# Kernel optimization log

Hardware: AMD Instinct MI355X
Metric: run time of the kernel (lower is better)

## Reference

```python
import jax, jax.numpy as jnp
import numpy as np

N_NODES = 50000
N_EDGES = 800000
IN_DIM = 128
HID = 64
HEADS = 4
OUT_DIM = 64
NEG_SLOPE = 0.2


def setup_inputs() -> dict:
    key = jax.random.key(0)
    ks = jax.random.split(key, 12)
    x = jax.random.normal(ks[0], (N_NODES, IN_DIM), dtype=jnp.float32)
    edge_index = jax.random.randint(ks[1], (2, N_EDGES), 0, N_NODES, dtype=jnp.int64)
    s = 0.1
    # GATConv layer 1: in_dim -> hid per head, 4 heads, concat
    W1 = jax.random.normal(ks[2], (IN_DIM, HEADS * HID), dtype=jnp.float32) * s
    a_src1 = jax.random.normal(ks[3], (HEADS, HID), dtype=jnp.float32) * s
    a_dst1 = jax.random.normal(ks[4], (HEADS, HID), dtype=jnp.float32) * s
    b1 = jnp.zeros((HEADS * HID,), dtype=jnp.float32)
    # GATConv layer 2: hid*heads -> out_dim, 1 head
    W2 = jax.random.normal(ks[5], (HEADS * HID, OUT_DIM), dtype=jnp.float32) * s
    a_src2 = jax.random.normal(ks[6], (1, OUT_DIM), dtype=jnp.float32) * s
    a_dst2 = jax.random.normal(ks[7], (1, OUT_DIM), dtype=jnp.float32) * s
    b2 = jnp.zeros((OUT_DIM,), dtype=jnp.float32)
    # final linear out_dim -> 1
    fc_w = jax.random.normal(ks[8], (OUT_DIM, 1), dtype=jnp.float32) * s
    fc_b = jnp.zeros((1,), dtype=jnp.float32)
    return {"x": x, "edge_index": edge_index, "W1": W1, "a_src1": a_src1,
            "a_dst1": a_dst1, "b1": b1, "W2": W2, "a_src2": a_src2,
            "a_dst2": a_dst2, "b2": b2, "fc_w": fc_w, "fc_b": fc_b}


def _gat_layer(x, src, dst, W, a_src, a_dst, bias, heads, out_c):
    """PyG-style GATConv: gather, edge attention, segment softmax, scatter-sum."""
    n = x.shape[0]
    h = (x @ W).reshape(n, heads, out_c)                    # [N,H,C]
    alpha_s = jnp.sum(h * a_src, axis=-1)                   # [N,H]
    alpha_d = jnp.sum(h * a_dst, axis=-1)                   # [N,H]
    e = jax.nn.leaky_relu(alpha_s[src] + alpha_d[dst], NEG_SLOPE)  # [E,H]
    # segment softmax over incoming edges of each destination node
    m = jax.ops.segment_max(e, dst, num_segments=n)         # [N,H]
    ex = jnp.exp(e - m[dst])
    den = jax.ops.segment_sum(ex, dst, num_segments=n)      # [N,H]
    alpha = ex / (den[dst] + 1e-16)                         # [E,H]
    out = jax.ops.segment_sum(alpha[:, :, None] * h[src], dst, num_segments=n)
    return out.reshape(n, heads * out_c) + bias


def reference(x, edge_index, W1, a_src1, a_dst1, b1, W2, a_src2, a_dst2, b2, fc_w, fc_b):
    n = x.shape[0]
    # GATConv default add_self_loops=True
    loop = jnp.arange(n, dtype=edge_index.dtype)
    src = jnp.concatenate([edge_index[0], loop])
    dst = jnp.concatenate([edge_index[1], loop])
    h = _gat_layer(x, src, dst, W1, a_src1, a_dst1, b1, HEADS, HID)
    h = jax.nn.elu(h)
    h = _gat_layer(h, src, dst, W2, a_src2, a_dst2, b2, 1, OUT_DIM)
    return jnp.squeeze(h @ fc_w + fc_b)                      # [N]
```

## Files before the change

### kernel.cpp

```cpp
#include <hip/hip_runtime.h>
#include <hip/hip_fp16.h>

#define N_NODES 50000
#define N_EDGES 800000
#define E_TOT   850000
#define IN_DIM  128
#define HID     64
#define HEADS   4
#define C1      256
#define OUT_DIM 64
#define NEG_SLOPE 0.2f

#define CP_NODES   32
#define CP_BLOCKS  ((N_NODES + CP_NODES - 1) / CP_NODES)
#define COUNT_BLOCKS ((E_TOT + 255) / 256)
#define NB_SCAN ((N_NODES + 255) / 256)

typedef __attribute__((ext_vector_type(8))) short v8s;
typedef __attribute__((ext_vector_type(4))) float v4f;

__device__ __forceinline__ unsigned int bf16_rne(float f) {
    unsigned int u = __float_as_uint(f);
    return (u + 0x7FFFu + ((u >> 16) & 1u)) >> 16;
}
__device__ __forceinline__ unsigned int bf16_pack2(float a, float b) {
    return bf16_rne(a) | (bf16_rne(b) << 16);
}
__device__ __forceinline__ float bf16_lo(unsigned int u) { return __uint_as_float(u << 16); }
__device__ __forceinline__ float bf16_hi(unsigned int u) { return __uint_as_float(u & 0xFFFF0000u); }

__device__ __forceinline__ unsigned int f16_pack2(float a, float b) {
    __half2 h = __floats2half2_rn(a, b);
    return *(unsigned int*)&h;
}
__device__ __forceinline__ float2 f16_unp2(unsigned int u) {
    __half2 h = *(__half2*)&u;
    return __half22float2(h);
}

__global__ __launch_bounds__(512) void prep_kernel(
    const float* __restrict__ W1, const float* __restrict__ a_src1,
    const float* __restrict__ a_dst1,
    const float* __restrict__ W2, const float* __restrict__ a_src2,
    const float* __restrict__ a_dst2, const float* __restrict__ b2,
    const float* __restrict__ fc_w, const float* __restrict__ fc_b,
    float* __restrict__ p_src, float* __restrict__ p_dst,
    float* __restrict__ v_s, float* __restrict__ v_d, float* __restrict__ v_z,
    float* __restrict__ cst, unsigned int* __restrict__ W1b)
{
    const int t = threadIdx.x;
    if (blockIdx.x > 0) {
        int idx = (blockIdx.x - 1) * 512 + t;
        int i    = idx & 3;
        int lane = (idx >> 2) & 63;
        int kk   = (idx >> 8) & 3;
        int nt   = (idx >> 10) & 3;
        int hh   = idx >> 12;
        int k0 = kk * 32 + (lane >> 4) * 8 + i * 2;
        int c  = hh * 64 + nt * 16 + (lane & 15);
        W1b[idx] = bf16_pack2(W1[(size_t)k0 * C1 + c], W1[(size_t)(k0 + 1) * C1 + c]);
        return;
    }
    const int k = t >> 2, h = t & 3;
    const float* wrow = W1 + k * C1 + h * HID;
    const float* as = a_src1 + h * HID;
    const float* ad = a_dst1 + h * HID;
    float s = 0.f, d = 0.f;
    for (int c = 0; c < HID; c++) {
        float w = wrow[c];
        s = fmaf(w, as[c], s);
        d = fmaf(w, ad[c], d);
    }
    p_src[k * HEADS + h] = s;
    p_dst[k * HEADS + h] = d;

    if (t < C1) {
        const float* w2row = W2 + t * OUT_DIM;
        float vs = 0.f, vd = 0.f, vz = 0.f;
        for (int c = 0; c < OUT_DIM; c++) {
            float w = w2row[c];
            vs = fmaf(w, a_src2[c], vs);
            vd = fmaf(w, a_dst2[c], vd);
            vz = fmaf(w, fc_w[c], vz);
        }
        v_s[t] = vs; v_d[t] = vd; v_z[t] = vz;
    }
    if (t == 0) {
        float s2 = 0.f;
        for (int c = 0; c < OUT_DIM; c++) s2 = fmaf(b2[c], fc_w[c], s2);
        cst[0] = s2 + fc_b[0];
    }
}

__global__ __launch_bounds__(256) void convproj_count_kernel(
    const float* __restrict__ x, const float* __restrict__ p_src,
    const float* __restrict__ p_dst, const int* __restrict__ dst_a,
    float* __restrict__ as1, float* __restrict__ ad1,
    unsigned int* __restrict__ xb, int* __restrict__ deg,
    int* __restrict__ posE)
{
    if (blockIdx.x >= CP_BLOCKS) {
        int j = (blockIdx.x - CP_BLOCKS) * 256 + threadIdx.x;
        if (j < E_TOT) {
            int d = (j < N_EDGES) ? dst_a[j] : (j - N_EDGES);
            posE[j] = atomicAdd(&deg[d], 1);
        }
        return;
    }
    __shared__ float ps[IN_DIM * HEADS];
    __shared__ float pd[IN_DIM * HEADS];
    const int t = threadIdx.x;
    for (int i = t; i < IN_DIM * HEADS; i += 256) { ps[i] = p_src[i]; pd[i] = p_dst[i]; }
    __syncthreads();
    const int wv   = t >> 6;
    const int lane = t & 63;
    float4 p0 = *(const float4*)(ps + (lane * 2) * HEADS);
    float4 p1 = *(const float4*)(ps + (lane * 2 + 1) * HEADS);
    float4 q0 = *(const float4*)(pd + (lane * 2) * HEADS);
    float4 q1 = *(const float4*)(pd + (lane * 2 + 1) * HEADS);
    const int nodeBase = blockIdx.x * CP_NODES + wv * 8;
    #pragma unroll
    for (int i = 0; i < 8; i++) {
        const int node = nodeBase + i;
        if (node >= N_NODES) break;
        float2 xv = *(const float2*)(x + (size_t)node * IN_DIM + lane * 2);
        xb[(size_t)node * 64 + lane] = bf16_pack2(xv.x, xv.y);
        float s0 = xv.x * p0.x + xv.y * p1.x;
        float s1 = xv.x * p0.y + xv.y * p1.y;
        float s2 = xv.x * p0.z + xv.y * p1.z;
        float s3 = xv.x * p0.w + xv.y * p1.w;
        float d0 = xv.x * q0.x + xv.y * q1.x;
        float d1 = xv.x * q0.y + xv.y * q1.y;
        float d2 = xv.x * q0.z + xv.y * q1.z;
        float d3 = xv.x * q0.w + xv.y * q1.w;
        #pragma unroll
        for (int off = 32; off; off >>= 1) {
            s0 += __shfl_down(s0, off, 64); s1 += __shfl_down(s1, off, 64);
            s2 += __shfl_down(s2, off, 64); s3 += __shfl_down(s3, off, 64);
            d0 += __shfl_down(d0, off, 64); d1 += __shfl_down(d1, off, 64);
            d2 += __shfl_down(d2, off, 64); d3 += __shfl_down(d3, off, 64);
        }
        if (lane == 0) {
            float4 sv = {s0, s1, s2, s3};
            float4 dv = {d0, d1, d2, d3};
            *(float4*)(as1 + node * 4) = sv;
            *(float4*)(ad1 + node * 4) = dv;
        }
    }
}

__global__ __launch_bounds__(256) void scanfuse_kernel(
    const int* __restrict__ deg, int* __restrict__ rowptr,
    int* aggP, int* incP)
{
    __shared__ int ps[256];
    __shared__ int bs[256];
    __shared__ int sprev;
    const int t = threadIdx.x;
    const int b = blockIdx.x;
    int i = b * 256 + t;
    int v = (i < N_NODES) ? deg[i] : 0;
    ps[t] = v;
    __syncthreads();
    for (int off = 1; off < 256; off <<= 1) {
        int u = (t >= off) ? ps[t - off] : 0;
        __syncthreads();
        ps[t] += u;
        __syncthreads();
    }
    if (t == 255) atomicExch(&aggP[b], ps[255] + 1);
    if (b == 0) {
        int val = 0;
        if (t < NB_SCAN) {
            while ((val = atomicAdd(&aggP[t], 0)) == 0) {}
            val -= 1;
        }
        bs[t] = (t < NB_SCAN) ? val : 0;
        __syncthreads();
        for (int off = 1; off < 256; off <<= 1) {
            int u = (t >= off) ? bs[t - off] : 0;
            __syncthreads();
            bs[t] += u;
            __syncthreads();
        }
        if (t < NB_SCAN) atomicExch(&incP[t], (bs[t] - val) + 1);
    }
    if (t == 0) {
        int val;
        while ((val = atomicAdd(&incP[b], 0)) == 0) {}
        sprev = val - 1;
    }
    __syncthreads();
    if (i <= N_NODES) rowptr[i] = sprev + ps[t] - v;
}

__global__ void fillw3_kernel(const int* __restrict__ src_a, const int* __restrict__ dst_a,
                              const int* __restrict__ rowptr, const int* __restrict__ posE,
                              const float* __restrict__ as1, const float* __restrict__ ad1,
                              int4* __restrict__ rec)
{
    int j = blockIdx.x * blockDim.x + threadIdx.x;
    if (j >= E_TOT) return;
    int s, d;
    if (j < N_EDGES) { s = src_a[j]; d = dst_a[j]; }
    else             { s = j - N_EDGES; d = s; }
    int slot = rowptr[d] + posE[j];
    float4 A  = *(const float4*)(as1 + s * 4);
    float4 Dv = *(const float4*)(ad1 + d * 4);
    float a0 = A.x + Dv.x, a1 = A.y + Dv.y, a2 = A.z + Dv.z, a3 = A.w + Dv.w;
    a0 = a0 > 0.f ? a0 : NEG_SLOPE * a0;
    a1 = a1 > 0.f ? a1 : NEG_SLOPE * a1;
    a2 = a2 > 0.f ? a2 : NEG_SLOPE * a2;
    a3 = a3 > 0.f ? a3 : NEG_SLOPE * a3;
    int4 r;
    r.x = s;
    r.y = (int)f16_pack2(__expf(a0), __expf(a1));
    r.z = (int)f16_pack2(__expf(a2), __expf(a3));
    r.w = 0;
    rec[slot] = r;
}

__global__ __launch_bounds__(256, 4) void agg1mlp_kernel(
    const int* __restrict__ rowptr, const int4* __restrict__ rec,
    const unsigned int* __restrict__ xb,
    const unsigned int* __restrict__ W1b, const float* __restrict__ b1,
    const float* __restrict__ v_s, const float* __restrict__ v_d,
    const float* __restrict__ v_z,
    float2* __restrict__ az, float* __restrict__ ad2)
{
    __shared__ unsigned int xsh[16 * 260];
    __shared__ float pr[4 * 16 * 3];
    const int t = threadIdx.x;
    const int nodeBase = blockIdx.x * 16;
    const int wv   = t >> 6;
    const int lane = t & 63;

    #pragma unroll 1
    for (int i = 0; i < 4; i++) {
        const int ln = wv * 4 + i;
        const int n  = nodeBase + ln;
        const int e0 = rowptr[n], e1 = rowptr[n + 1];

        float2 acc0 = {0,0}, acc1 = {0,0}, acc2 = {0,0}, acc3 = {0,0};
        float den0 = 0, den1 = 0, den2 = 0, den3 = 0;
        int e = e0;

        #pragma unroll 1
        for (; e + 8 <= e1; e += 8) {
            int4 r[8];
            #pragma unroll
            for (int k = 0; k < 8; k++) r[k] = rec[e + k];
            unsigned int xu[8];
            #pragma unroll
            for (int k = 0; k < 8; k++)
                xu[k] = xb[((unsigned)r[k].x << 6) + lane];
            #pragma unroll
            for (int k = 0; k < 8; k++) {
                float2 Wa = f16_unp2(r[k].y), Wb = f16_unp2(r[k].z);
                float xa = bf16_lo(xu[k]), xbv = bf16_hi(xu[k]);
                acc0.x = fmaf(Wa.x, xa, acc0.x); acc0.y = fmaf(Wa.x, xbv, acc0.y);
                acc1.x = fmaf(Wa.y, xa, acc1.x); acc1.y = fmaf(Wa.y, xbv, acc1.y);
                acc2.x = fmaf(Wb.x, xa, acc2.x); acc2.y = fmaf(Wb.x, xbv, acc2.y);
                acc3.x = fmaf(Wb.y, xa, acc3.x); acc3.y = fmaf(Wb.y, xbv, acc3.y);
                den0 += Wa.x; den1 += Wa.y; den2 += Wb.x; den3 += Wb.y;
            }
        }
        if (e + 4 <= e1) {
            int4 r[4];
            #pragma unroll
            for (int k = 0; k < 4; k++) r[k] = rec[e + k];
            unsigned int xu[4];
            #pragma unroll
            for (int k = 0; k < 4; k++)
                xu[k] = xb[((unsigned)r[k].x << 6) + lane];
            #pragma unroll
            for (int k = 0; k < 4; k++) {
                float2 Wa = f16_unp2(r[k].y), Wb = f16_unp2(r[k].z);
                float xa = bf16_lo(xu[k]), xbv = bf16_hi(xu[k]);
                acc0.x = fmaf(Wa.x, xa, acc0.x); acc0.y = fmaf(Wa.x, xbv, acc0.y);
                acc1.x = fmaf(Wa.y, xa, acc1.x); acc1.y = fmaf(Wa.y, xbv, acc1.y);
                acc2.x = fmaf(Wb.x, xa, acc2.x); acc2.y = fmaf(Wb.x, xbv, acc2.y);
                acc3.x = fmaf(Wb.y, xa, acc3.x); acc3.y = fmaf(Wb.y, xbv, acc3.y);
                den0 += Wa.x; den1 += Wa.y; den2 += Wb.x; den3 += Wb.y;
            }
            e += 4;
        }
        for (; e < e1; e++) {
            int4 r0 = rec[e];
            unsigned int xu = xb[((unsigned)r0.x << 6) + lane];
            float2 Wa = f16_unp2(r0.y), Wb = f16_unp2(r0.z);
            float xa = bf16_lo(xu), xbv = bf16_hi(xu);
            acc0.x = fmaf(Wa.x, xa, acc0.x); acc0.y = fmaf(Wa.x, xbv, acc0.y);
            acc1.x = fmaf(Wa.y, xa, acc1.x); acc1.y = fmaf(Wa.y, xbv, acc1.y);
            acc2.x = fmaf(Wb.x, xa, acc2.x); acc2.y = fmaf(Wb.x, xbv, acc2.y);
            acc3.x = fmaf(Wb.y, xa, acc3.x); acc3.y = fmaf(Wb.y, xbv, acc3.y);
            den0 += Wa.x; den1 += Wa.y; den2 += Wb.x; den3 += Wb.y;
        }
        float i0 = 1.f / (den0 + 1e-16f), i1 = 1.f / (den1 + 1e-16f);
        float i2 = 1.f / (den2 + 1e-16f), i3 = 1.f / (den3 + 1e-16f);
        unsigned int* o = xsh + ln * 260 + lane;
        o[0 * 64] = bf16_pack2(acc0.x * i0, acc0.y * i0);
        o[1 * 64] = bf16_pack2(acc1.x * i1, acc1.y * i1);
        o[2 * 64] = bf16_pack2(acc2.x * i2, acc2.y * i2);
        o[3 * 64] = bf16_pack2(acc3.x * i3, acc3.y * i3);
    }
    __syncthreads();

    {
        const int h = wv;
        const int m = lane & 15, quad = lane >> 4;
        const unsigned int* abase = xsh + m * 260 + h * 64 + quad * 4;
        v8s af0 = *(const v8s*)(abase + 0);
        v8s af1 = *(const v8s*)(abase + 16);
        v8s af2 = *(const v8s*)(abase + 32);
        v8s af3 = *(const v8s*)(abase + 48);

        float Sr[4] = {0,0,0,0}, Dr[4] = {0,0,0,0}, Zr[4] = {0,0,0,0};
        #pragma unroll
        for (int nt = 0; nt < 4; nt++) {
            const unsigned int* bbase = W1b + (size_t)(h * 16 + nt * 4) * 256 + lane * 4;
            v4f acc = {0.f, 0.f, 0.f, 0.f};
            acc = __builtin_amdgcn_mfma_f32_16x16x32_bf16(af0, *(const v8s*)(bbase + 0 * 256), acc, 0, 0, 0);
            acc = __builtin_amdgcn_mfma_f32_16x16x32_bf16(af1, *(const v8s*)(bbase + 1 * 256), acc, 0, 0, 0);
            acc = __builtin_amdgcn_mfma_f32_16x16x32_bf16(af2, *(const v8s*)(bbase + 2 * 256), acc, 0, 0, 0);
            acc = __builtin_amdgcn_mfma_f32_16x16x32_bf16(af3, *(const v8s*)(bbase + 3 * 256), acc, 0, 0, 0);
            const int c = h * 64 + nt * 16 + m;
            float bb = b1[c], vsc = v_s[c], vdc = v_d[c], vzc = v_z[c];
            #pragma unroll
            for (int r = 0; r < 4; r++) {
                float o = acc[r] + bb;
                o = o > 0.f ? o : __expf(o) - 1.f;
                Sr[r] = fmaf(o, vsc, Sr[r]);
                Dr[r] = fmaf(o, vdc, Dr[r]);
                Zr[r] = fmaf(o, vzc, Zr[r]);
            }
        }
        #pragma unroll
        for (int off = 8; off; off >>= 1) {
            #pragma unroll
            for (int r = 0; r < 4; r++) {
                Sr[r] += __shfl_down(Sr[r], off, 16);
                Dr[r] += __shfl_down(Dr[r], off, 16);
                Zr[r] += __shfl_down(Zr[r], off, 16);
            }
        }
        if (m == 0) {
            #pragma unroll
            for (int r = 0; r < 4; r++) {
                const int row = quad * 4 + r;
                pr[(h * 16 + row) * 3 + 0] = Sr[r];
                pr[(h * 16 + row) * 3 + 1] = Dr[r];
                pr[(h * 16 + row) * 3 + 2] = Zr[r];
            }
        }
    }
    __syncthreads();

    if (t < 16) {
        float s = 0.f, d = 0.f, z = 0.f;
        #pragma unroll
        for (int w = 0; w < 4; w++) {
            s += pr[(w * 16 + t) * 3 + 0];
            d += pr[(w * 16 + t) * 3 + 1];
            z += pr[(w * 16 + t) * 3 + 2];
        }
        const int node = nodeBase + t;
        float2 azv = {s, z};
        az[node]  = azv;
        ad2[node] = d;
    }
}

__global__ __launch_bounds__(256) void agg2z_kernel(
    const int* __restrict__ rowptr, const int4* __restrict__ rec,
    const float2* __restrict__ az, const float* __restrict__ ad2,
    const float* __restrict__ cst, float* __restrict__ out)
{
    int gid  = blockIdx.x * blockDim.x + threadIdx.x;
    int n    = gid >> 4;
    int sl   = threadIdx.x & 15;
    if (n >= N_NODES) return;
    const float adh = ad2[n];
    const int e0 = rowptr[n], e1 = rowptr[n + 1];

    float acc = 0.f, den = 0.f;
    for (int e = e0 + sl; e < e1; e += 16) {
        int s = rec[e].x;
        float2 v = az[s];
        float a = v.x + adh;
        a = a > 0.f ? a : NEG_SLOPE * a;
        float w = __expf(a);
        acc = fmaf(w, v.y, acc);
        den += w;
    }
    #pragma unroll
    for (int off = 8; off; off >>= 1) {
        acc += __shfl_down(acc, off, 16);
        den += __shfl_down(den, off, 16);
    }
    if (sl == 0) out[n] = acc / (den + 1e-16f) + cst[0];
}

extern "C" void kernel_launch(void* const* d_in, const int* in_sizes, int n_in,
                              void* d_out, int out_size, void* d_ws, size_t ws_size,
                              hipStream_t stream)
{
    const float* x      = (const float*)d_in[0];
    const int*   ei     = (const int*)d_in[1];
    const float* W1     = (const float*)d_in[2];
    const float* a_src1 = (const float*)d_in[3];
    const float* a_dst1 = (const float*)d_in[4];
    const float* b1     = (const float*)d_in[5];
    const float* W2     = (const float*)d_in[6];
    const float* a_src2 = (const float*)d_in[7];
    const float* a_dst2 = (const float*)d_in[8];
    const float* b2     = (const float*)d_in[9];
    const float* fc_w   = (const float*)d_in[10];
    const float* fc_b   = (const float*)d_in[11];
    float* out = (float*)d_out;

    const int* srcA = ei;
    const int* dstA = ei + N_EDGES;

    float* ws = (float*)d_ws;
    size_t off = 0;
    unsigned int* xb    = (unsigned int*)(ws + off); off += (size_t)N_NODES * 64;
    int4* rec      = (int4*)(ws + off); off += (size_t)E_TOT * 4 + 256;
    int* posE      = (int*)(ws + off); off += E_TOT + 256;
    float* as1     = ws + off; off += (size_t)N_NODES * HEADS;
    float* ad1     = ws + off; off += (size_t)N_NODES * HEADS;
    float2* az     = (float2*)(ws + off); off += (size_t)N_NODES * 2;
    float* ad2     = ws + off; off += N_NODES;
    float* p_src   = ws + off; off += IN_DIM * HEADS;
    float* p_dst   = ws + off; off += IN_DIM * HEADS;
    float* v_s     = ws + off; off += C1;
    float* v_d     = ws + off; off += C1;
    float* v_z     = ws + off; off += C1;
    float* cst     = ws + off; off += 2;
    unsigned int* W1b = (unsigned int*)(ws + off); off += 16384;
    int* rowptr    = (int*)(ws + off); off += N_NODES + 1 + 256;
    int* aggP      = (int*)(ws + off); off += 256;
    int* incP      = (int*)(ws + off); off += 256;
    int* deg       = (int*)(ws + off); off += N_NODES;
    hipMemsetAsync(aggP, 0, (512 + N_NODES) * sizeof(int), stream);

    prep_kernel<<<33, 512, 0, stream>>>(W1, a_src1, a_dst1, W2, a_src2, a_dst2,
                                        b2, fc_w, fc_b, p_src, p_dst, v_s, v_d, v_z, cst, W1b);

    convproj_count_kernel<<<CP_BLOCKS + COUNT_BLOCKS, 256, 0, stream>>>(
        x, p_src, p_dst, dstA, as1, ad1, xb, deg, posE);

    scanfuse_kernel<<<NB_SCAN, 256, 0, stream>>>(deg, rowptr, aggP, incP);

    fillw3_kernel<<<COUNT_BLOCKS, 256, 0, stream>>>(srcA, dstA, rowptr, posE,
                                                    as1, ad1, rec);

    agg1mlp_kernel<<<N_NODES / 16, 256, 0, stream>>>(rowptr, rec, xb, W1b, b1,
                                                     v_s, v_d, v_z, az, ad2);

    agg2z_kernel<<<(N_NODES * 16 + 255) / 256, 256, 0, stream>>>(rowptr, rec, az, ad2, cst, out);
}
```

Baseline: 250.1 us.

## Compute layer-1 edge attention weights inside aggregation instead of precomputed records

The CSR fill kernel now writes only source indices (4 bytes per edge) instead of 16-byte records holding f16-packed exp attention weights. The layer-1 aggregation kernel gathers the source node's alpha_src float4, adds the destination alpha_dst, and computes leaky-relu and exp on the fly. The 4-edge tail block is dropped. This cuts fill-kernel work and record traffic in both aggregation kernels, at the cost of an extra random float4 gather and four exps per edge in every lane of the wave, which repeats work across 64 lanes.

```diff
diff --git a/kernel.cpp b/kernel.cpp
--- a/kernel.cpp
+++ b/kernel.cpp
@@ -28,15 +28,6 @@
 }
 __device__ __forceinline__ float bf16_lo(unsigned int u) { return __uint_as_float(u << 16); }
 __device__ __forceinline__ float bf16_hi(unsigned int u) { return __uint_as_float(u & 0xFFFF0000u); }
-
-__device__ __forceinline__ unsigned int f16_pack2(float a, float b) {
-    __half2 h = __floats2half2_rn(a, b);
-    return *(unsigned int*)&h;
-}
-__device__ __forceinline__ float2 f16_unp2(unsigned int u) {
-    __half2 h = *(__half2*)&u;
-    return __half22float2(h);
-}
 
 __global__ __launch_bounds__(512) void prep_kernel(
     const float* __restrict__ W1, const float* __restrict__ a_src1,
@@ -194,34 +185,21 @@
     if (i <= N_NODES) rowptr[i] = sprev + ps[t] - v;
 }
 
-__global__ void fillw3_kernel(const int* __restrict__ src_a, const int* __restrict__ dst_a,
-                              const int* __restrict__ rowptr, const int* __restrict__ posE,
-                              const float* __restrict__ as1, const float* __restrict__ ad1,
-                              int4* __restrict__ rec)
+__global__ void fillsrc_kernel(const int* __restrict__ src_a, const int* __restrict__ dst_a,
+                               const int* __restrict__ rowptr, const int* __restrict__ posE,
+                               int* __restrict__ srcs)
 {
     int j = blockIdx.x * blockDim.x + threadIdx.x;
     if (j >= E_TOT) return;
     int s, d;
     if (j < N_EDGES) { s = src_a[j]; d = dst_a[j]; }
     else             { s = j - N_EDGES; d = s; }
-    int slot = rowptr[d] + posE[j];
-    float4 A  = *(const float4*)(as1 + s * 4);
-    float4 Dv = *(const float4*)(ad1 + d * 4);
-    float a0 = A.x + Dv.x, a1 = A.y + Dv.y, a2 = A.z + Dv.z, a3 = A.w + Dv.w;
-    a0 = a0 > 0.f ? a0 : NEG_SLOPE * a0;
-    a1 = a1 > 0.f ? a1 : NEG_SLOPE * a1;
-    a2 = a2 > 0.f ? a2 : NEG_SLOPE * a2;
-    a3 = a3 > 0.f ? a3 : NEG_SLOPE * a3;
-    int4 r;
-    r.x = s;
-    r.y = (int)f16_pack2(__expf(a0), __expf(a1));
-    r.z = (int)f16_pack2(__expf(a2), __expf(a3));
-    r.w = 0;
-    rec[slot] = r;
+    srcs[rowptr[d] + posE[j]] = s;
 }
 
 __global__ __launch_bounds__(256, 4) void agg1mlp_kernel(
-    const int* __restrict__ rowptr, const int4* __restrict__ rec,
+    const int* __restrict__ rowptr, const int* __restrict__ srcs,
+    const float4* __restrict__ as1v, const float4* __restrict__ ad1v,
     const unsigned int* __restrict__ xb,
     const unsigned int* __restrict__ W1b, const float* __restrict__ b1,
     const float* __restrict__ v_s, const float* __restrict__ v_d,
@@ -240,6 +218,7 @@
         const int ln = wv * 4 + i;
         const int n  = nodeBase + ln;
         const int e0 = rowptr[n], e1 = rowptr[n + 1];
+        const float4 D = ad1v[n];
 
         float2 acc0 = {0,0}, acc1 = {0,0}, acc2 = {0,0}, acc3 = {0,0};
         float den0 = 0, den1 = 0, den2 = 0, den3 = 0;
@@ -247,54 +226,50 @@
 
         #pragma unroll 1
         for (; e + 8 <= e1; e += 8) {
-            int4 r[8];
-            #pragma unroll
-            for (int k = 0; k < 8; k++) r[k] = rec[e + k];
+            int sidx[8];
+            #pragma unroll
+            for (int k = 0; k < 8; k++) sidx[k] = srcs[e + k];
             unsigned int xu[8];
             #pragma unroll
             for (int k = 0; k < 8; k++)
-                xu[k] = xb[((unsigned)r[k].x << 6) + lane];
+                xu[k] = xb[((unsigned)sidx[k] << 6) + lane];
             #pragma unroll
             for (int k = 0; k < 8; k++) {
-                float2 Wa = f16_unp2(r[k].y), Wb = f16_unp2(r[k].z);
+                float4 A = as1v[sidx[k]];
+                float a0 = A.x + D.x, a1 = A.y + D.y;
+                float a2 = A.z + D.z, a3 = A.w + D.w;
+                a0 = a0 > 0.f ? a0 : NEG_SLOPE * a0;
+                a1 = a1 > 0.f ? a1 : NEG_SLOPE * a1;
+                a2 = a2 > 0.f ? a2 : NEG_SLOPE * a2;
+                a3 = a3 > 0.f ? a3 : NEG_SLOPE * a3;
+                float w0 = __expf(a0), w1 = __expf(a1);
+                float w2 = __expf(a2), w3 = __expf(a3);
                 float xa = bf16_lo(xu[k]), xbv = bf16_hi(xu[k]);
-                acc0.x = fmaf(Wa.x, xa, acc0.x); acc0.y = fmaf(Wa.x, xbv, acc0.y);
-                acc1.x = fmaf(Wa.y, xa, acc1.x); acc1.y = fmaf(Wa.y, xbv, acc1.y);
-                acc2.x = fmaf(Wb.x, xa, acc2.x); acc2.y = fmaf(Wb.x, xbv, acc2.y);
-                acc3.x = fmaf(Wb.y, xa, acc3.x); acc3.y = fmaf(Wb.y, xbv, acc3.y);
-                den0 += Wa.x; den1 += Wa.y; den2 += Wb.x; den3 += Wb.y;
+                acc0.x = fmaf(w0, xa, acc0.x); acc0.y = fmaf(w0, xbv, acc0.y);
+                acc1.x = fmaf(w1, xa, acc1.x); acc1.y = fmaf(w1, xbv, acc1.y);
+                acc2.x = fmaf(w2, xa, acc2.x); acc2.y = fmaf(w2, xbv, acc2.y);
+                acc3.x = fmaf(w3, xa, acc3.x); acc3.y = fmaf(w3, xbv, acc3.y);
+                den0 += w0; den1 += w1; den2 += w2; den3 += w3;
             }
         }
-        if (e + 4 <= e1) {
-            int4 r[4];
-            #pragma unroll
-            for (int k = 0; k < 4; k++) r[k] = rec[e + k];
-            unsigned int xu[4];
-            #pragma unroll
-            for (int k = 0; k < 4; k++)
-                xu[k] = xb[((unsigned)r[k].x << 6) + lane];
-            #pragma unroll
-            for (int k = 0; k < 4; k++) {
-                float2 Wa = f16_unp2(r[k].y), Wb = f16_unp2(r[k].z);
-                float xa = bf16_lo(xu[k]), xbv = bf16_hi(xu[k]);
-                acc0.x = fmaf(Wa.x, xa, acc0.x); acc0.y = fmaf(Wa.x, xbv, acc0.y);
-                acc1.x = fmaf(Wa.y, xa, acc1.x); acc1.y = fmaf(Wa.y, xbv, acc1.y);
-                acc2.x = fmaf(Wb.x, xa, acc2.x); acc2.y = fmaf(Wb.x, xbv, acc2.y);
-                acc3.x = fmaf(Wb.y, xa, acc3.x); acc3.y = fmaf(Wb.y, xbv, acc3.y);
-                den0 += Wa.x; den1 += Wa.y; den2 += Wb.x; den3 += Wb.y;
-            }
-            e += 4;
-        }
         for (; e < e1; e++) {
-            int4 r0 = rec[e];
-            unsigned int xu = xb[((unsigned)r0.x << 6) + lane];
-            float2 Wa = f16_unp2(r0.y), Wb = f16_unp2(r0.z);
+            int s0 = srcs[e];
+            unsigned int xu = xb[((unsigned)s0 << 6) + lane];
+            float4 A = as1v[s0];
+            float a0 = A.x + D.x, a1 = A.y + D.y;
+            float a2 = A.z + D.z, a3 = A.w + D.w;
+            a0 = a0 > 0.f ? a0 : NEG_SLOPE * a0;
+            a1 = a1 > 0.f ? a1 : NEG_SLOPE * a1;
+            a2 = a2 > 0.f ? a2 : NEG_SLOPE * a2;
+            a3 = a3 > 0.f ? a3 : NEG_SLOPE * a3;
+            float w0 = __expf(a0), w1 = __expf(a1);
+            float w2 = __expf(a2), w3 = __expf(a3);
             float xa = bf16_lo(xu), xbv = bf16_hi(xu);
-            acc0.x = fmaf(Wa.x, xa, acc0.x); acc0.y = fmaf(Wa.x, xbv, acc0.y);
-            acc1.x = fmaf(Wa.y, xa, acc1.x); acc1.y = fmaf(Wa.y, xbv, acc1.y);
-            acc2.x = fmaf(Wb.x, xa, acc2.x); acc2.y = fmaf(Wb.x, xbv, acc2.y);
-            acc3.x = fmaf(Wb.y, xa, acc3.x); acc3.y = fmaf(Wb.y, xbv, acc3.y);
-            den0 += Wa.x; den1 += Wa.y; den2 += Wb.x; den3 += Wb.y;
+            acc0.x = fmaf(w0, xa, acc0.x); acc0.y = fmaf(w0, xbv, acc0.y);
+            acc1.x = fmaf(w1, xa, acc1.x); acc1.y = fmaf(w1, xbv, acc1.y);
+            acc2.x = fmaf(w2, xa, acc2.x); acc2.y = fmaf(w2, xbv, acc2.y);
+            acc3.x = fmaf(w3, xa, acc3.x); acc3.y = fmaf(w3, xbv, acc3.y);
+            den0 += w0; den1 += w1; den2 += w2; den3 += w3;
         }
         float i0 = 1.f / (den0 + 1e-16f), i1 = 1.f / (den1 + 1e-16f);
         float i2 = 1.f / (den2 + 1e-16f), i3 = 1.f / (den3 + 1e-16f);
@@ -372,7 +347,7 @@
 }
 
 __global__ __launch_bounds__(256) void agg2z_kernel(
-    const int* __restrict__ rowptr, const int4* __restrict__ rec,
+    const int* __restrict__ rowptr, const int* __restrict__ srcs,
     const float2* __restrict__ az, const float* __restrict__ ad2,
     const float* __restrict__ cst, float* __restrict__ out)
 {
@@ -385,7 +360,7 @@
 
     float acc = 0.f, den = 0.f;
     for (int e = e0 + sl; e < e1; e += 16) {
-        int s = rec[e].x;
+        int s = srcs[e];
         float2 v = az[s];
         float a = v.x + adh;
         a = a > 0.f ? a : NEG_SLOPE * a;
@@ -425,7 +400,7 @@
     float* ws = (float*)d_ws;
     size_t off = 0;
     unsigned int* xb    = (unsigned int*)(ws + off); off += (size_t)N_NODES * 64;
-    int4* rec      = (int4*)(ws + off); off += (size_t)E_TOT * 4 + 256;
+    int* srcs      = (int*)(ws + off); off += E_TOT + 256;
     int* posE      = (int*)(ws + off); off += E_TOT + 256;
     float* as1     = ws + off; off += (size_t)N_NODES * HEADS;
     float* ad1     = ws + off; off += (size_t)N_NODES * HEADS;
@@ -452,11 +427,11 @@
 
     scanfuse_kernel<<<NB_SCAN, 256, 0, stream>>>(deg, rowptr, aggP, incP);
 
-    fillw3_kernel<<<COUNT_BLOCKS, 256, 0, stream>>>(srcA, dstA, rowptr, posE,
-                                                    as1, ad1, rec);
-
-    agg1mlp_kernel<<<N_NODES / 16, 256, 0, stream>>>(rowptr, rec, xb, W1b, b1,
-                                                     v_s, v_d, v_z, az, ad2);
-
-    agg2z_kernel<<<(N_NODES * 16 + 255) / 256, 256, 0, stream>>>(rowptr, rec, az, ad2, cst, out);
-}
+    fillsrc_kernel<<<COUNT_BLOCKS, 256, 0, stream>>>(srcA, dstA, rowptr, posE, srcs);
+
+    agg1mlp_kernel<<<N_NODES / 16, 256, 0, stream>>>(rowptr, srcs,
+                                                     (const float4*)as1, (const float4*)ad1,
+                                                     xb, W1b, b1, v_s, v_d, v_z, az, ad2);
+
+    agg2z_kernel<<<(N_NODES * 16 + 255) / 256, 256, 0, stream>>>(rowptr, srcs, az, ad2, cst, out);
+}
```

Result: slower. 279.8 us (+11.9%).
